# Performance work log

Hardware: AMD Instinct MI355X
Metric: run time of the kernel (lower is better)

The kernel has to match this reference:

```python
import jax, jax.numpy as jnp
import numpy as np

# Model config (matches init_kwargs)
DAG_DEPTH = 16
HIDDEN = 2048
B, T = 4, 4096
N = DAG_DEPTH                 # total_nodes
INIT_SLOTS = DAG_DEPTH // 2   # initial slots
INTER = DAG_DEPTH // 2        # intermediate slots / scan steps
LOG_CLAMP = 23.026
SIGN_TEMP = 1e-4


def _xavier(k, shape):
    fan_out, fan_in = shape
    lim = np.sqrt(6.0 / (fan_in + fan_out)).astype(np.float32)
    return jax.random.uniform(k, shape, jnp.float32, -lim, lim)


def setup_inputs() -> dict:
    key = jax.random.key(0)
    k0, k1, k2, k3 = jax.random.split(key, 4)
    return {
        "hidden": jax.random.normal(k0, (B, T, HIDDEN), jnp.float32),
        "W_init": _xavier(k1, (2 * N, HIDDEN)),
        "b_init": jnp.zeros((2 * N,), jnp.float32),
        "W_op": _xavier(k2, (INTER * N, HIDDEN)),
        "b_op": jnp.zeros((INTER * N,), jnp.float32),
        "W_gate": _xavier(k3, (INTER, HIDDEN)),
        "b_gate": jnp.zeros((INTER,), jnp.float32),
    }


def reference(hidden, W_init, b_init, W_op, b_op, W_gate, b_gate):
    Bb, Tt, H = hidden.shape
    # --- plan predictor ---
    init_raw = jnp.einsum('bth,oh->bto', hidden, W_init) + b_init        # (B,T,2N)
    V_mag = jnp.abs(init_raw[..., :N])                                   # (B,T,N)
    V_sign = jnp.tanh(init_raw[..., N:])                                 # (B,T,N)
    O = (jnp.einsum('bth,oh->bto', hidden, W_op) + b_op).reshape(Bb, Tt, INTER, N)
    G = jax.nn.sigmoid(jnp.einsum('bth,oh->bto', hidden, W_gate) + b_gate)  # (B,T,INTER)

    # --- sequential DAG execution (fixed INTER steps, vectorized over B,T) ---
    # NOTE: torch casts to float64 (float32 on mps); here we compute in float32,
    # identical math modulo precision (jax x64 is disabled by default).
    pos = jnp.arange(N)
    for step in range(INTER):
        valid = INIT_SLOTS + step
        mask = (pos < valid).astype(hidden.dtype)                        # causal mask over nodes
        O_s = O[:, :, step, :] * mask                                    # (B,T,N)
        G_s = G[:, :, step:step + 1]                                     # (B,T,1)
        signed = V_sign * V_mag
        log_mag = jnp.log(jnp.clip(V_mag, 1e-12))
        mixed = log_mag * (1.0 - G_s) + signed * G_s
        R = jnp.sum(O_s * mixed, axis=-1, keepdims=True)                 # (B,T,1)
        lin_sign = jnp.tanh(R / SIGN_TEMP)
        sign_prod = jnp.prod(V_sign * (jnp.abs(O_s) + 1.0), axis=-1, keepdims=True)
        log_sign = jnp.tanh(sign_prod / SIGN_TEMP)
        Vs_new = G_s * lin_sign + (1.0 - G_s) * log_sign
        Vm_new = G_s * jnp.abs(R) + (1.0 - G_s) * jnp.exp(jnp.clip(R, None, LOG_CLAMP))
        idx = INIT_SLOTS + step
        V_mag = V_mag.at[:, :, idx].set(Vm_new[..., 0])
        V_sign = V_sign.at[:, :, idx].set(Vs_new[..., 0])

    return V_sign[:, :, -1] * V_mag[:, :, -1]                            # (B,T)
```

## Files before the change

### kernel.cpp

```cpp
#include <hip/hip_runtime.h>
#include <math.h>

#define HID    2048
#define NROW   16384
#define NCOL   168
#define BM     32
#define KSTEPS 64
#define NELEM  2112
#define BUFB   33792
#define CPD    172
#define NSLOT  16
#define NSTEP  8

typedef short short8 __attribute__((ext_vector_type(8)));
typedef float f32x4  __attribute__((ext_vector_type(4)));
typedef unsigned int u32x4 __attribute__((ext_vector_type(4)));

static __device__ __forceinline__ void wait_vm13() {
  asm volatile("s_waitcnt vmcnt(13)" ::: "memory");
}
static __device__ __forceinline__ void wait_vm0() {
  asm volatile("s_waitcnt vmcnt(0)" ::: "memory");
}
static __device__ __forceinline__ void wait_lgkm0() {
  asm volatile("s_waitcnt lgkmcnt(0)" ::: "memory");
}

static __device__ __forceinline__ unsigned pack_hi(unsigned u0, unsigned u1) {
  return __builtin_amdgcn_perm(u1, u0, 0x07060302u);
}

struct Planes { u32x4 p1, p2, p3; };
static __device__ __forceinline__ Planes split8(const float* x) {
  Planes P;
  #pragma unroll
  for (int q = 0; q < 4; ++q) {
    float x0 = x[2*q], x1 = x[2*q+1];
    unsigned u0 = __float_as_uint(x0), u1 = __float_as_uint(x1);
    P.p1[q] = pack_hi(u0, u1);
    float r0 = x0 - __uint_as_float(u0 & 0xFFFF0000u);
    float r1 = x1 - __uint_as_float(u1 & 0xFFFF0000u);
    unsigned v0 = __float_as_uint(r0), v1 = __float_as_uint(r1);
    P.p2[q] = pack_hi(v0, v1);
    float s0 = r0 - __uint_as_float(v0 & 0xFFFF0000u);
    float s1 = r1 - __uint_as_float(v1 & 0xFFFF0000u);
    P.p3[q] = pack_hi(__float_as_uint(s0), __float_as_uint(s1));
  }
  return P;
}

static __device__ __forceinline__ void loadA8(const float* p, float* x) {
  f32x4 a = *(const f32x4*)p;
  f32x4 b = *(const f32x4*)(p + 4);
  x[0]=a[0]; x[1]=a[1]; x[2]=a[2]; x[3]=a[3];
  x[4]=b[0]; x[5]=b[1]; x[6]=b[2]; x[7]=b[3];
}

static __device__ __forceinline__ f32x4 mf(short8 a, short8 b, f32x4 c) {
  return __builtin_amdgcn_mfma_f32_16x16x32_bf16(a, b, c, 0, 0, 0);
}

static __device__ __forceinline__ void gld_lds16(const void* g, void* l) {
  __builtin_amdgcn_global_load_lds(
      (const __attribute__((address_space(1))) unsigned int*)g,
      (__attribute__((address_space(3))) unsigned int*)l, 16, 0, 0);
}

__global__ void prep_b(const float* __restrict__ Wi, const float* __restrict__ Wo,
                       const float* __restrict__ Wg, u32x4* __restrict__ wsB) {
  int bid  = blockIdx.x;
  int kidx = bid / 11;
  int nt   = bid - kidx * 11;
  int l    = threadIdx.x;
  int col  = nt * 16 + (l & 15);
  int k0   = kidx * 32 + (l >> 4) * 8;

  float x[8];
  if (col < NCOL) {
    const float* wr = (col < 32)  ? (Wi + (size_t)col * HID)
                    : (col < 160) ? (Wo + (size_t)(col - 32) * HID)
                                  : (Wg + (size_t)(col - 160) * HID);
    loadA8(wr + k0, x);
  } else {
    #pragma unroll
    for (int i = 0; i < 8; ++i) x[i] = 0.f;
  }
  Planes P = split8(x);
  size_t base = (size_t)kidx * NELEM + (nt * 3) * 64 + l;
  wsB[base]       = P.p1;
  wsB[base + 64]  = P.p2;
  wsB[base + 128] = P.p3;
}

__global__ __launch_bounds__(256, 2)
void dag_main(const float* __restrict__ hidden, const u32x4* __restrict__ wsB,
              const float* __restrict__ b_init, const float* __restrict__ b_op,
              const float* __restrict__ b_gate, float* __restrict__ out)
{
  __shared__ __align__(16) char smem[2 * BUFB];

  const int tid = threadIdx.x;
  const int l   = tid & 63;
  const int w   = tid >> 6;
  const int row0 = blockIdx.x * BM;
  const int r   = l & 15;
  const int kg  = l >> 4;

  const float* ap0 = hidden + (size_t)(row0 + r) * HID + kg * 8;
  const float* ap1 = ap0 + (size_t)16 * HID;

  const u32x4* gsrc[9];
  char* ldst[9];
  #pragma unroll
  for (int i = 0; i < 9; ++i) {
    int ii = (w == 3 && i >= 6) ? i - 6 : i;
    int c  = 9 * w + ii;
    gsrc[i] = wsB + (size_t)c * 64 + l;
    ldst[i] = smem + c * 1024;
  }
  const char* brd0 = smem + (size_t)(9 * w) * 1024 + (size_t)l * 16;

  f32x4 acc[2][3];
  const f32x4 zf = {0.f, 0.f, 0.f, 0.f};
  #pragma unroll
  for (int mt = 0; mt < 2; ++mt)
    #pragma unroll
    for (int j = 0; j < 3; ++j) acc[mt][j] = zf;

  float xa0[8], xa1[8], xb0[8], xb1[8];

#define STAGE(t_, sel_) do {                                                \
    _Pragma("unroll")                                                       \
    for (int i = 0; i < 9; ++i)                                             \
      gld_lds16(gsrc[i] + (size_t)NELEM * (t_), ldst[i] + (sel_) * BUFB);   \
  } while (0)

#define BODY(t_, p_, xc0_, xc1_, ISSUE_, LAST_) do {                        \
    if (LAST_) wait_vm0(); else wait_vm13();                                \
    __builtin_amdgcn_sched_barrier(0);                                      \
    const char* bb = brd0 + (p_) * BUFB;                                    \
    short8 bf[9];                                                           \
    _Pragma("unroll")                                                       \
    for (int i = 0; i < 9; ++i)                                             \
      if (w != 3 || i < 6) bf[i] = *(const short8*)(bb + i * 1024);         \
    wait_lgkm0();     \
    __builtin_amdgcn_sched_barrier(0);                                      \
    if (ISSUE_) STAGE((t_) + 2, (p_));                                      \
    Planes PA0 = split8(xc0_);                                              \
    Planes PA1 = split8(xc1_);                                              \
    if (ISSUE_) {                                                           \
      loadA8(ap0 + ((t_) + 2) * 32, xc0_);                                  \
      loadA8(ap1 + ((t_) + 2) * 32, xc1_);                                  \
    }                                                                       \
    short8 a0p1 = __builtin_bit_cast(short8, PA0.p1);                       \
    short8 a0p2 = __builtin_bit_cast(short8, PA0.p2);                       \
    short8 a0p3 = __builtin_bit_cast(short8, PA0.p3);                       \
    short8 a1p1 = __builtin_bit_cast(short8, PA1.p1);                       \
    short8 a1p2 = __builtin_bit_cast(short8, PA1.p2);                       \
    short8 a1p3 = __builtin_bit_cast(short8, PA1.p3);                       \
    __builtin_amdgcn_s_setprio(1);                                          \
    _Pragma("unroll")                                                       \
    for (int j = 0; j < 3; ++j) {                                           \
      if (w == 3 && j == 2) continue;                                       \
      short8 b1 = bf[j * 3 + 0];                                            \
      short8 b2 = bf[j * 3 + 1];                                            \
      short8 b3 = bf[j * 3 + 2];                                            \
      {                                                                     \
        f32x4 c = acc[0][j];                                                \
        c = mf(a0p1, b1, c); c = mf(a0p1, b2, c); c = mf(a0p2, b1, c);      \
        c = mf(a0p1, b3, c); c = mf(a0p2, b2, c); c = mf(a0p3, b1, c);      \
        acc[0][j] = c;                                                      \
      }                                                                     \
      {                                                                     \
        f32x4 c = acc[1][j];                                                \
        c = mf(a1p1, b1, c); c = mf(a1p1, b2, c); c = mf(a1p2, b1, c);      \
        c = mf(a1p1, b3, c); c = mf(a1p2, b2, c); c = mf(a1p3, b1, c);      \
        acc[1][j] = c;                                                      \
      }                                                                     \
    }                                                                       \
    __builtin_amdgcn_s_setprio(0);                                          \
  } while (0)

  STAGE(0, 0);
  loadA8(ap0,      xa0);
  loadA8(ap1,      xa1);
  STAGE(1, 1);
  loadA8(ap0 + 32, xb0);
  loadA8(ap1 + 32, xb1);

  for (int t = 0; t < 62; t += 2) {
    BODY(t,     0, xa0, xa1, true, false);
    BODY(t + 1, 1, xb0, xb1, true, false);
  }
  BODY(62, 0, xa0, xa1, false, false);
  BODY(63, 1, xb0, xb1, false, true);
#undef BODY
#undef STAGE

  __syncthreads();
  float (*sC)[CPD] = (float(*)[CPD])smem;
  #pragma unroll
  for (int mt = 0; mt < 2; ++mt) {
    #pragma unroll
    for (int j = 0; j < 3; ++j) {
      int col = w * 48 + j * 16 + r;
      if (col < NCOL) {
        int row = mt * 16 + kg * 4;
        sC[row + 0][col] = acc[mt][j][0];
        sC[row + 1][col] = acc[mt][j][1];
        sC[row + 2][col] = acc[mt][j][2];
        sC[row + 3][col] = acc[mt][j][3];
      }
    }
  }
  __syncthreads();

  if (tid < BM) {
    const int rr = tid;
    float Vm[NSLOT], Vs[NSLOT];
    #pragma unroll
    for (int i = 0; i < NSLOT; ++i) {
      float mv = sC[rr][i]      + b_init[i];
      float sv = sC[rr][16 + i] + b_init[16 + i];
      Vm[i] = fabsf(mv);
      Vs[i] = tanhf(sv);
    }
    float G[NSTEP];
    #pragma unroll
    for (int s = 0; s < NSTEP; ++s) {
      float gr = sC[rr][160 + s] + b_gate[s];
      G[s] = 1.0f / (1.0f + expf(-gr));
    }
    #pragma unroll
    for (int s = 0; s < NSTEP; ++s) {
      const float g = G[s];
      float R = 0.f, sp = 1.f;
      #pragma unroll
      for (int i = 0; i < NSLOT; ++i) {
        float Osi = (i < 8 + s) ? (sC[rr][32 + s * 16 + i] + b_op[s * 16 + i]) : 0.f;
        float sgn   = Vs[i] * Vm[i];
        float logm  = logf(fmaxf(Vm[i], 1e-12f));
        float mixed = logm * (1.f - g) + sgn * g;
        R  += Osi * mixed;
        sp *= Vs[i] * (fabsf(Osi) + 1.f);
      }
      float lin_sign = tanhf(R  / 1e-4f);
      float log_sign = tanhf(sp / 1e-4f);
      float vs_new = g * lin_sign + (1.f - g) * log_sign;
      float vm_new = g * fabsf(R) + (1.f - g) * expf(fminf(R, 23.026f));
      Vm[8 + s] = vm_new;
      Vs[8 + s] = vs_new;
    }
    out[row0 + rr] = Vs[NSLOT - 1] * Vm[NSLOT - 1];
  }
}

extern "C" void kernel_launch(void* const* d_in, const int* in_sizes, int n_in,
                              void* d_out, int out_size, void* d_ws, size_t ws_size,
                              hipStream_t stream) {
  (void)in_sizes; (void)n_in; (void)out_size; (void)ws_size;
  const float* hidden = (const float*)d_in[0];
  const float* W_init = (const float*)d_in[1];
  const float* b_init = (const float*)d_in[2];
  const float* W_op   = (const float*)d_in[3];
  const float* b_op   = (const float*)d_in[4];
  const float* W_gate = (const float*)d_in[5];
  const float* b_gate = (const float*)d_in[6];
  float* out = (float*)d_out;
  u32x4* wsB = (u32x4*)d_ws;

  prep_b<<<dim3(704), dim3(64), 0, stream>>>(W_init, W_op, W_gate, wsB);
  dag_main<<<dim3(NROW / BM), dim3(256), 0, stream>>>(hidden, wsB, b_init, b_op,
                                                      b_gate, out);
}
```

Measured before the change: 115.3 us.

## Double row tile with 8 waves sharing B tiles via triple-buffered LDS

Doubles the row block to 64 with 512 threads, so two wave groups share each staged B (weight) tile and the cooperative global-to-LDS loads are split across all eight waves. LDS buffering moves from double to triple, and per-wave waits plus lgkm waits are replaced with a block-wide s_barrier each k-step. The aim is to halve weight traffic per row and spread load issue across more waves. In exchange it adds a barrier per step and roughly 100KB of LDS per block, which may limit occupancy, and the epilogue shared-memory C buffer must now hold 64 rows.

```diff
diff --git a/kernel.cpp b/kernel.cpp
--- a/kernel.cpp
+++ b/kernel.cpp
@@ -4,7 +4,7 @@
 #define HID    2048
 #define NROW   16384
 #define NCOL   168
-#define BM     32
+#define BM     64
 #define KSTEPS 64
 #define NELEM  2112
 #define BUFB   33792
@@ -16,14 +16,11 @@
 typedef float f32x4  __attribute__((ext_vector_type(4)));
 typedef unsigned int u32x4 __attribute__((ext_vector_type(4)));
 
-static __device__ __forceinline__ void wait_vm13() {
-  asm volatile("s_waitcnt vmcnt(13)" ::: "memory");
+static __device__ __forceinline__ void wait_vm9() {
+  asm volatile("s_waitcnt vmcnt(9)" ::: "memory");
 }
 static __device__ __forceinline__ void wait_vm0() {
   asm volatile("s_waitcnt vmcnt(0)" ::: "memory");
-}
-static __device__ __forceinline__ void wait_lgkm0() {
-  asm volatile("s_waitcnt lgkmcnt(0)" ::: "memory");
 }
 
 static __device__ __forceinline__ unsigned pack_hi(unsigned u0, unsigned u1) {
@@ -92,33 +89,34 @@
   wsB[base + 128] = P.p3;
 }
 
-__global__ __launch_bounds__(256, 2)
+__global__ __launch_bounds__(512, 2)
 void dag_main(const float* __restrict__ hidden, const u32x4* __restrict__ wsB,
               const float* __restrict__ b_init, const float* __restrict__ b_op,
               const float* __restrict__ b_gate, float* __restrict__ out)
 {
-  __shared__ __align__(16) char smem[2 * BUFB];
+  __shared__ __align__(16) char smem[3 * BUFB];
 
   const int tid = threadIdx.x;
   const int l   = tid & 63;
   const int w   = tid >> 6;
+  const int wn  = w & 3;
+  const int wm  = w >> 2;
   const int row0 = blockIdx.x * BM;
   const int r   = l & 15;
   const int kg  = l >> 4;
 
-  const float* ap0 = hidden + (size_t)(row0 + r) * HID + kg * 8;
+  const float* ap0 = hidden + (size_t)(row0 + wm * 32 + r) * HID + kg * 8;
   const float* ap1 = ap0 + (size_t)16 * HID;
 
-  const u32x4* gsrc[9];
-  char* ldst[9];
-  #pragma unroll
-  for (int i = 0; i < 9; ++i) {
-    int ii = (w == 3 && i >= 6) ? i - 6 : i;
-    int c  = 9 * w + ii;
-    gsrc[i] = wsB + (size_t)c * 64 + l;
-    ldst[i] = smem + c * 1024;
-  }
-  const char* brd0 = smem + (size_t)(9 * w) * 1024 + (size_t)l * 16;
+  const int cb = 9 * wn + (wm ? ((wn == 3) ? 1 : 4) : 0);
+  const u32x4* gsrc[5];
+  char* ldst[5];
+  #pragma unroll
+  for (int i = 0; i < 5; ++i) {
+    gsrc[i] = wsB + (size_t)(cb + i) * 64 + l;
+    ldst[i] = smem + (cb + i) * 1024;
+  }
+  const char* brd0 = smem + (size_t)(9 * wn) * 1024 + (size_t)l * 16;
 
   f32x4 acc[2][3];
   const f32x4 zf = {0.f, 0.f, 0.f, 0.f};
@@ -131,21 +129,21 @@
 
 #define STAGE(t_, sel_) do {                                                \
     _Pragma("unroll")                                                       \
-    for (int i = 0; i < 9; ++i)                                             \
+    for (int i = 0; i < 5; ++i)                                             \
       gld_lds16(gsrc[i] + (size_t)NELEM * (t_), ldst[i] + (sel_) * BUFB);   \
   } while (0)
 
 #define BODY(t_, p_, xc0_, xc1_, ISSUE_, LAST_) do {                        \
-    if (LAST_) wait_vm0(); else wait_vm13();                                \
+    if (LAST_) wait_vm0(); else wait_vm9();                                 \
+    __builtin_amdgcn_sched_barrier(0);                                      \
+    __builtin_amdgcn_s_barrier();                                           \
     __builtin_amdgcn_sched_barrier(0);                                      \
     const char* bb = brd0 + (p_) * BUFB;                                    \
     short8 bf[9];                                                           \
     _Pragma("unroll")                                                       \
     for (int i = 0; i < 9; ++i)                                             \
-      if (w != 3 || i < 6) bf[i] = *(const short8*)(bb + i * 1024);         \
-    wait_lgkm0();     \
-    __builtin_amdgcn_sched_barrier(0);                                      \
-    if (ISSUE_) STAGE((t_) + 2, (p_));                                      \
+      if (wn != 3 || i < 6) bf[i] = *(const short8*)(bb + i * 1024);        \
+    if (ISSUE_) STAGE((t_) + 2, ((p_) + 2) % 3);                            \
     Planes PA0 = split8(xc0_);                                              \
     Planes PA1 = split8(xc1_);                                              \
     if (ISSUE_) {                                                           \
@@ -161,7 +159,7 @@
     __builtin_amdgcn_s_setprio(1);                                          \
     _Pragma("unroll")                                                       \
     for (int j = 0; j < 3; ++j) {                                           \
-      if (w == 3 && j == 2) continue;                                       \
+      if (wn == 3 && j == 2) continue;                                      \
       short8 b1 = bf[j * 3 + 0];                                            \
       short8 b2 = bf[j * 3 + 1];                                            \
       short8 b3 = bf[j * 3 + 2];                                            \
@@ -188,12 +186,18 @@
   loadA8(ap0 + 32, xb0);
   loadA8(ap1 + 32, xb1);
 
-  for (int t = 0; t < 62; t += 2) {
-    BODY(t,     0, xa0, xa1, true, false);
+  for (int t = 0; t < 60; t += 6) {
+    BODY(t + 0, 0, xa0, xa1, true, false);
     BODY(t + 1, 1, xb0, xb1, true, false);
-  }
-  BODY(62, 0, xa0, xa1, false, false);
-  BODY(63, 1, xb0, xb1, false, true);
+    BODY(t + 2, 2, xa0, xa1, true, false);
+    BODY(t + 3, 0, xb0, xb1, true, false);
+    BODY(t + 4, 1, xa0, xa1, true, false);
+    BODY(t + 5, 2, xb0, xb1, true, false);
+  }
+  BODY(60, 0, xa0, xa1, true,  false);
+  BODY(61, 1, xb0, xb1, true,  false);
+  BODY(62, 2, xa0, xa1, false, false);
+  BODY(63, 0, xb0, xb1, false, true);
 #undef BODY
 #undef STAGE
 
@@ -203,9 +207,9 @@
   for (int mt = 0; mt < 2; ++mt) {
     #pragma unroll
     for (int j = 0; j < 3; ++j) {
-      int col = w * 48 + j * 16 + r;
+      int col = wn * 48 + j * 16 + r;
       if (col < NCOL) {
-        int row = mt * 16 + kg * 4;
+        int row = wm * 32 + mt * 16 + kg * 4;
         sC[row + 0][col] = acc[mt][j][0];
         sC[row + 1][col] = acc[mt][j][1];
         sC[row + 2][col] = acc[mt][j][2];
@@ -270,6 +274,6 @@
   u32x4* wsB = (u32x4*)d_ws;
 
   prep_b<<<dim3(704), dim3(64), 0, stream>>>(W_init, W_op, W_gate, wsB);
-  dag_main<<<dim3(NROW / BM), dim3(256), 0, stream>>>(hidden, wsB, b_init, b_op,
+  dag_main<<<dim3(NROW / BM), dim3(512), 0, stream>>>(hidden, wsB, b_init, b_op,
                                                       b_gate, out);
 }
```

New measurement: 100.5 us. -12.8%, faster.
